# Performance work log

Measured on AMD Instinct MI355X. Metric: run time of the kernel, lower is better.

## Reference

```python
import jax, jax.numpy as jnp
import numpy as np

T, C, A = 8192, 512, 64  # context_length, embedding_size, attention_size
EPS = 1e-5


def setup_inputs() -> dict:
    key = jax.random.key(0)
    ks = jax.random.split(key, 5)
    x = jax.random.normal(ks[0], (T, C), dtype=jnp.float32)
    x_emb = jax.random.normal(ks[1], (T, C), dtype=jnp.float32)
    Wq = jax.random.normal(ks[2], (C, A), dtype=jnp.float32) / np.sqrt(C)
    Wk = jax.random.normal(ks[3], (C, A), dtype=jnp.float32) / np.sqrt(C)
    Wv = jax.random.normal(ks[4], (C, C), dtype=jnp.float32) / np.sqrt(C)
    return {
        "x": x,
        "x_emb": x_emb,
        "ln_scale": jnp.ones((C,), jnp.float32),
        "ln_bias": jnp.zeros((C,), jnp.float32),
        "Wq": Wq,
        "Wk": Wk,
        "Wv": Wv,
    }


def _layernorm(x, scale, bias):
    mu = jnp.mean(x, axis=-1, keepdims=True)
    var = jnp.mean(jnp.square(x - mu), axis=-1, keepdims=True)
    return (x - mu) * jax.lax.rsqrt(var + EPS) * scale + bias


def reference(x, x_emb, ln_scale, ln_bias, Wq, Wk, Wv):
    t = x.shape[0]
    xx = _layernorm(x, ln_scale, ln_bias)            # [T, C]
    q = xx @ Wq                                       # [T, A]
    k = xx @ Wk                                       # [T, A]
    c = jnp.einsum('ta,sa->ts', q, k) * (A ** -0.5)  # [T, T]
    # causal tril mask; masked positions set to 0 (NO softmax in this module)
    mask = jnp.tril(jnp.ones((t, t), dtype=bool))
    c = jnp.where(mask, c, 0.0)
    v = x_emb @ Wv                                    # [T, C]
    return x + c @ v
```

## Files before the change

kernel.cpp:

```cpp
#include <hip/hip_runtime.h>

#define TT 8192
#define CC 512

typedef unsigned short u16;
typedef unsigned int u32;
typedef __attribute__((ext_vector_type(8))) short bf16x8;
typedef __attribute__((ext_vector_type(4))) float f32x4;

#define VMCNT0() asm volatile("s_waitcnt vmcnt(0)" ::: "memory")
#define LGKM0()  asm volatile("s_waitcnt lgkmcnt(0)" ::: "memory")

__device__ __forceinline__ u16 f2bf(float f) {
    u32 u = __float_as_uint(f);
    return (u16)((u + 0x7FFFu + ((u >> 16) & 1u)) >> 16);
}

__device__ __forceinline__ void gld16(const u16* g, u16* l) {
    __builtin_amdgcn_global_load_lds(
        (const __attribute__((address_space(1))) u32*)g,
        (__attribute__((address_space(3))) u32*)l, 16, 0, 0);
}

__global__ void lnw_kernel(const float* __restrict__ x,
                           const float* __restrict__ scale,
                           const float* __restrict__ bias,
                           const float* __restrict__ Wq,
                           const float* __restrict__ Wk,
                           const float* __restrict__ Wv,
                           const float* __restrict__ xe,
                           u16* __restrict__ xx,
                           u16* __restrict__ wqkt,
                           u16* __restrict__ wvt,
                           u16* __restrict__ xeb) {
    int b = blockIdx.x;
    if (b < 2048) {
        int row = b * 4 + (threadIdx.x >> 6);
        int l = threadIdx.x & 63;
        const float4* xr = (const float4*)(x + (size_t)row * CC);
        float4 a = xr[l * 2], c = xr[l * 2 + 1];
        float s = a.x + a.y + a.z + a.w + c.x + c.y + c.z + c.w;
        float q = a.x*a.x + a.y*a.y + a.z*a.z + a.w*a.w
                + c.x*c.x + c.y*c.y + c.z*c.z + c.w*c.w;
        #pragma unroll
        for (int m = 1; m < 64; m <<= 1) {
            s += __shfl_xor(s, m, 64);
            q += __shfl_xor(q, m, 64);
        }
        float mu = s * (1.0f / CC);
        float var = q * (1.0f / CC) - mu * mu;
        float rs = rsqrtf(var + 1e-5f);
        const float4* sc4 = (const float4*)scale;
        const float4* bi4 = (const float4*)bias;
        float4 s1 = sc4[l * 2], s2 = sc4[l * 2 + 1];
        float4 b1 = bi4[l * 2], b2 = bi4[l * 2 + 1];
        bf16x8 o;
        o[0] = (short)f2bf((a.x - mu) * rs * s1.x + b1.x);
        o[1] = (short)f2bf((a.y - mu) * rs * s1.y + b1.y);
        o[2] = (short)f2bf((a.z - mu) * rs * s1.z + b1.z);
        o[3] = (short)f2bf((a.w - mu) * rs * s1.w + b1.w);
        o[4] = (short)f2bf((c.x - mu) * rs * s2.x + b2.x);
        o[5] = (short)f2bf((c.y - mu) * rs * s2.y + b2.y);
        o[6] = (short)f2bf((c.z - mu) * rs * s2.z + b2.z);
        o[7] = (short)f2bf((c.w - mu) * rs * s2.w + b2.w);
        *(bf16x8*)(xx + (size_t)row * CC + l * 8) = o;
    } else if (b < 3328) {
        int tid = (b - 2048) * 256 + threadIdx.x;
        if (tid < 65536) {
            int c = tid >> 9, k = tid & 511;
            float w = (c < 64) ? Wq[k * 64 + c] * 0.125f : Wk[k * 64 + (c - 64)];
            wqkt[tid] = f2bf(w);
        } else {
            int i = tid - 65536;
            int c = i >> 9, k = i & 511;
            wvt[i] = f2bf(Wv[k * 512 + c]);
        }
    } else {
        size_t i = (size_t)(b - 3328) * 2048 + (size_t)threadIdx.x * 8;
        float4 a = *(const float4*)(xe + i);
        float4 c = *(const float4*)(xe + i + 4);
        bf16x8 o;
        o[0] = (short)f2bf(a.x); o[1] = (short)f2bf(a.y);
        o[2] = (short)f2bf(a.z); o[3] = (short)f2bf(a.w);
        o[4] = (short)f2bf(c.x); o[5] = (short)f2bf(c.y);
        o[6] = (short)f2bf(c.z); o[7] = (short)f2bf(c.w);
        *(bf16x8*)(xeb + i) = o;
    }
}

__global__ __launch_bounds__(512, 4) void qkv_gemm_kernel(const u16* __restrict__ xx,
                                                          const u16* __restrict__ wqkt,
                                                          const u16* __restrict__ xeb,
                                                          const u16* __restrict__ wvt,
                                                          u16* __restrict__ qk,
                                                          u16* __restrict__ kt,
                                                          u16* __restrict__ vt) {
    extern __shared__ u16 smem[];

    const int tid = threadIdx.x;
    const int w = tid >> 6, l = tid & 63;
    const int l15 = l & 15, g = l >> 4;
    const int wr = w >> 2, wc = w & 3;

    const bool isqk = blockIdx.x < 64;
    int r0, c0;
    const u16 *Asrc, *Bsrc;
    if (isqk) { r0 = blockIdx.x * 128; c0 = 0; Asrc = xx; Bsrc = wqkt; }
    else {
        int b2 = blockIdx.x - 64;
        r0 = (b2 >> 2) * 128; c0 = (b2 & 3) * 128; Asrc = xeb; Bsrc = wvt;
    }

    const int drow = tid >> 3, sl = tid & 7;
    #define A_DMA(KK, B) { \
        _Pragma("unroll") \
        for (int i = 0; i < 2; ++i) { \
            int r = i * 64 + drow; \
            gld16(Asrc + (size_t)(r0 + r) * CC + (KK) * 64 + ((sl ^ (r & 7)) << 3), \
                  smem + (B) * 8192 + r * 64 + sl * 8); \
        } }
    #define B_DMA(KK, B) { \
        _Pragma("unroll") \
        for (int i = 0; i < 2; ++i) { \
            int r = i * 64 + drow; \
            gld16(Bsrc + (size_t)(c0 + r) * CC + (KK) * 64 + ((sl ^ (r & 7)) << 3), \
                  smem + 16384 + (B) * 8192 + r * 64 + sl * 8); \
        } }

    f32x4 acc[4][2];
    #pragma unroll
    for (int m = 0; m < 4; ++m)
        #pragma unroll
        for (int n = 0; n < 2; ++n) acc[m][n] = (f32x4){0.f, 0.f, 0.f, 0.f};

    A_DMA(0, 0); B_DMA(0, 0);

    int cur = 0;
    for (int kk = 0; kk < 8; ++kk) {
        VMCNT0();
        LGKM0();
        __builtin_amdgcn_s_barrier();
        if (kk < 7) { A_DMA(kk + 1, cur ^ 1); B_DMA(kk + 1, cur ^ 1); }

        const u16* Ab = smem + cur * 8192;
        const u16* Bb = smem + 16384 + cur * 8192;
        __builtin_amdgcn_s_setprio(1);
        #pragma unroll
        for (int ka = 0; ka < 2; ++ka) {
            bf16x8 af[4], bfr[2];
            #pragma unroll
            for (int Mt = 0; Mt < 4; ++Mt) {
                int r = wr * 64 + Mt * 16 + l15;
                int ph = (ka * 4 + g) ^ (r & 7);
                af[Mt] = *(const bf16x8*)&Ab[r * 64 + ph * 8];
            }
            #pragma unroll
            for (int Nt = 0; Nt < 2; ++Nt) {
                int c = wc * 32 + Nt * 16 + l15;
                int ph = (ka * 4 + g) ^ (c & 7);
                bfr[Nt] = *(const bf16x8*)&Bb[c * 64 + ph * 8];
            }
            #pragma unroll
            for (int Mt = 0; Mt < 4; ++Mt)
                #pragma unroll
                for (int Nt = 0; Nt < 2; ++Nt)
                    acc[Mt][Nt] = __builtin_amdgcn_mfma_f32_16x16x32_bf16(af[Mt], bfr[Nt], acc[Mt][Nt], 0, 0, 0);
        }
        __builtin_amdgcn_s_setprio(0);
        cur ^= 1;
    }

    if (isqk) {
        #pragma unroll
        for (int Mt = 0; Mt < 4; ++Mt) {
            #pragma unroll
            for (int Nt = 0; Nt < 2; ++Nt) {
                int col = wc * 32 + Nt * 16 + l15;
                #pragma unroll
                for (int jj = 0; jj < 4; ++jj) {
                    int row = wr * 64 + Mt * 16 + g * 4 + jj;
                    qk[(size_t)(r0 + row) * 128 + col] = f2bf(acc[Mt][Nt][jj]);
                }
            }
        }
        __syncthreads();
        u16* tl = smem;
        if (wc >= 2) {
            #pragma unroll
            for (int Mt = 0; Mt < 4; ++Mt) {
                #pragma unroll
                for (int Nt = 0; Nt < 2; ++Nt) {
                    int a = (wc - 2) * 32 + Nt * 16 + l15;
                    #pragma unroll
                    for (int jj = 0; jj < 4; ++jj) {
                        int row = wr * 64 + Mt * 16 + g * 4 + jj;
                        tl[a * 136 + row] = f2bf(acc[Mt][Nt][jj]);
                    }
                }
            }
        }
        __syncthreads();
        #pragma unroll
        for (int i = 0; i < 2; ++i) {
            int chunk = i * 512 + tid;
            int a = chunk >> 4, r8 = chunk & 15;
            *(bf16x8*)(kt + (size_t)a * TT + r0 + r8 * 8) = *(const bf16x8*)&tl[a * 136 + r8 * 8];
        }
    } else {
        __syncthreads();
        u16* tl = smem;
        #pragma unroll
        for (int Mt = 0; Mt < 4; ++Mt) {
            #pragma unroll
            for (int Nt = 0; Nt < 2; ++Nt) {
                int col = wc * 32 + Nt * 16 + l15;
                #pragma unroll
                for (int jj = 0; jj < 4; ++jj) {
                    int row = wr * 64 + Mt * 16 + g * 4 + jj;
                    tl[col * 136 + row] = f2bf(acc[Mt][Nt][jj]);
                }
            }
        }
        __syncthreads();
        #pragma unroll
        for (int i = 0; i < 4; ++i) {
            int chunk = i * 512 + tid;
            int c = chunk >> 4, r8 = chunk & 15;
            *(bf16x8*)(vt + (size_t)(c0 + c) * TT + r0 + r8 * 8) = *(const bf16x8*)&tl[c * 136 + r8 * 8];
        }
    }
    #undef A_DMA
    #undef B_DMA
}

__global__ __launch_bounds__(512) void gkv_kernel(const u16* __restrict__ vt,
                                                  const u16* __restrict__ kt,
                                                  float* __restrict__ H) {
    int m = blockIdx.x >> 2, cq = blockIdx.x & 3;
    int w = threadIdx.x >> 6, l = threadIdx.x & 63;
    int l15 = l & 15, g = l >> 4;
    int c0 = cq * 128 + (w >> 1) * 32;
    int a0 = (w & 1) * 32;

    f32x4 acc[2][2];
    #pragma unroll
    for (int i = 0; i < 2; ++i)
        #pragma unroll
        for (int n = 0; n < 2; ++n) acc[i][n] = (f32x4){0.f, 0.f, 0.f, 0.f};

    #pragma unroll
    for (int ka = 0; ka < 4; ++ka) {
        int k = m * 128 + ka * 32 + g * 8;
        bf16x8 af[2], bfr[2];
        #pragma unroll
        for (int Mt = 0; Mt < 2; ++Mt)
            af[Mt] = *(const bf16x8*)(vt + (size_t)(c0 + Mt * 16 + l15) * TT + k);
        #pragma unroll
        for (int Nt = 0; Nt < 2; ++Nt)
            bfr[Nt] = *(const bf16x8*)(kt + (size_t)(a0 + Nt * 16 + l15) * TT + k);
        #pragma unroll
        for (int Mt = 0; Mt < 2; ++Mt)
            #pragma unroll
            for (int Nt = 0; Nt < 2; ++Nt)
                acc[Mt][Nt] = __builtin_amdgcn_mfma_f32_16x16x32_bf16(af[Mt], bfr[Nt], acc[Mt][Nt], 0, 0, 0);
    }

    float* hp = H + (size_t)m * 32768;
    #pragma unroll
    for (int Mt = 0; Mt < 2; ++Mt) {
        #pragma unroll
        for (int Nt = 0; Nt < 2; ++Nt) {
            int a = a0 + Nt * 16 + l15;
            #pragma unroll
            for (int jj = 0; jj < 4; ++jj) {
                int c = c0 + Mt * 16 + g * 4 + jj;
                hp[c * 64 + a] = acc[Mt][Nt][jj];
            }
        }
    }
}

__global__ __launch_bounds__(256) void scanA_kernel(const float* __restrict__ H,
                                                    float* __restrict__ Asum) {
    int idx = blockIdx.x * 256 + threadIdx.x;
    int g = idx >> 15, e = idx & 32767;
    float s = 0.f;
    #pragma unroll
    for (int t = 0; t < 8; ++t) s += H[(size_t)(8 * g + t) * 32768 + e];
    Asum[(size_t)g * 32768 + e] = s;
}

__global__ __launch_bounds__(256) void scanB_kernel(const float* __restrict__ H,
                                                    const float* __restrict__ Asum,
                                                    u16* __restrict__ ptb) {
    int idx = blockIdx.x * 256 + threadIdx.x;
    int g = idx >> 15, e = idx & 32767;
    float acc = 0.f;
    for (int g2 = 0; g2 < g; ++g2) acc += Asum[(size_t)g2 * 32768 + e];
    ptb[(size_t)(8 * g) * 32768 + e] = f2bf(acc);
    #pragma unroll
    for (int t = 1; t < 8; ++t) {
        acc += H[(size_t)(8 * g + t - 1) * 32768 + e];
        ptb[(size_t)(8 * g + t) * 32768 + e] = f2bf(acc);
    }
}

__global__ __launch_bounds__(512) void out_kernel(const u16* __restrict__ qk,
                                                  const u16* __restrict__ ptb,
                                                  const u16* __restrict__ vt,
                                                  const float* __restrict__ x,
                                                  float* __restrict__ out) {
    __shared__ u16 Slds[128 * 128];

    const int tid = threadIdx.x;
    const int w = tid >> 6, l = tid & 63;
    const int l15 = l & 15, g = l >> 4;
    const int wr = w >> 2, wcol = w & 3;

    const int rt = (int)blockIdx.x >> 2;
    const int cb = (int)blockIdx.x & 3;

    f32x4 acc[4][2];
    #pragma unroll
    for (int m = 0; m < 4; ++m)
        #pragma unroll
        for (int n = 0; n < 2; ++n) acc[m][n] = (f32x4){0.f, 0.f, 0.f, 0.f};

    const int dq = rt * 128 + w * 16 + l15;
    const bf16x8 qa0 = *(const bf16x8*)(qk + (size_t)dq * 128 + g * 8);
    const bf16x8 qa1 = *(const bf16x8*)(qk + (size_t)dq * 128 + 32 + g * 8);
    #pragma unroll
    for (int Nt = 0; Nt < 8; ++Nt) {
        int scol = Nt * 16 + l15;
        f32x4 sacc = (f32x4){0.f, 0.f, 0.f, 0.f};
        #pragma unroll
        for (int ka = 0; ka < 2; ++ka) {
            bf16x8 kf = *(const bf16x8*)(qk + (size_t)(rt * 128 + scol) * 128 + 64 + ka * 32 + g * 8);
            sacc = __builtin_amdgcn_mfma_f32_16x16x32_bf16(ka ? qa1 : qa0, kf, sacc, 0, 0, 0);
        }
        #pragma unroll
        for (int jj = 0; jj < 4; ++jj) {
            int row = w * 16 + g * 4 + jj;
            float val = (scol > row) ? 0.f : sacc[jj];
            int slot = (scol >> 3) ^ (row & 15);
            Slds[row * 128 + slot * 8 + (scol & 7)] = f2bf(val);
        }
    }

    #pragma unroll
    for (int ka = 0; ka < 2; ++ka) {
        bf16x8 qf[4], pf[2];
        #pragma unroll
        for (int Mt = 0; Mt < 4; ++Mt)
            qf[Mt] = *(const bf16x8*)(qk + (size_t)(rt * 128 + wr * 64 + Mt * 16 + l15) * 128 + ka * 32 + g * 8);
        #pragma unroll
        for (int Nt = 0; Nt < 2; ++Nt) {
            int c = cb * 128 + wcol * 32 + Nt * 16 + l15;
            pf[Nt] = *(const bf16x8*)(ptb + (size_t)rt * 32768 + c * 64 + ka * 32 + g * 8);
        }
        #pragma unroll
        for (int Mt = 0; Mt < 4; ++Mt)
            #pragma unroll
            for (int Nt = 0; Nt < 2; ++Nt)
                acc[Mt][Nt] = __builtin_amdgcn_mfma_f32_16x16x32_bf16(qf[Mt], pf[Nt], acc[Mt][Nt], 0, 0, 0);
    }

    __syncthreads();

    #pragma unroll
    for (int ks = 0; ks < 4; ++ks) {
        bf16x8 sf[4], vf[2];
        #pragma unroll
        for (int Mt = 0; Mt < 4; ++Mt) {
            int row = wr * 64 + Mt * 16 + l15;
            int slot = (ks * 4 + g) ^ (row & 15);
            sf[Mt] = *(const bf16x8*)&Slds[row * 128 + slot * 8];
        }
        #pragma unroll
        for (int Nt = 0; Nt < 2; ++Nt) {
            int c = cb * 128 + wcol * 32 + Nt * 16 + l15;
            vf[Nt] = *(const bf16x8*)(vt + (size_t)c * TT + rt * 128 + ks * 32 + g * 8);
        }
        #pragma unroll
        for (int Mt = 0; Mt < 4; ++Mt)
            #pragma unroll
            for (int Nt = 0; Nt < 2; ++Nt)
                acc[Mt][Nt] = __builtin_amdgcn_mfma_f32_16x16x32_bf16(sf[Mt], vf[Nt], acc[Mt][Nt], 0, 0, 0);
    }

    #pragma unroll
    for (int Mt = 0; Mt < 4; ++Mt) {
        #pragma unroll
        for (int Nt = 0; Nt < 2; ++Nt) {
            int col = cb * 128 + wcol * 32 + Nt * 16 + l15;
            #pragma unroll
            for (int jj = 0; jj < 4; ++jj) {
                int row = rt * 128 + wr * 64 + Mt * 16 + g * 4 + jj;
                out[(size_t)row * 512 + col] = x[(size_t)row * 512 + col] + acc[Mt][Nt][jj];
            }
        }
    }
}

extern "C" void kernel_launch(void* const* d_in, const int* in_sizes, int n_in,
                              void* d_out, int out_size, void* d_ws, size_t ws_size,
                              hipStream_t stream) {
    (void)in_sizes; (void)n_in; (void)out_size; (void)ws_size;
    const float* x    = (const float*)d_in[0];
    const float* xe   = (const float*)d_in[1];
    const float* lns  = (const float*)d_in[2];
    const float* lnb  = (const float*)d_in[3];
    const float* Wq   = (const float*)d_in[4];
    const float* Wk   = (const float*)d_in[5];
    const float* Wv   = (const float*)d_in[6];
    float* out = (float*)d_out;
    char* ws = (char*)d_ws;

    size_t off_xx   = 0;
    size_t off_qk   = off_xx   + (size_t)TT * CC * 2;
    size_t off_wqkt = off_qk   + (size_t)TT * 128 * 2;
    size_t off_wvt  = off_wqkt + (size_t)128 * 512 * 2;
    size_t off_vt   = off_wvt  + (size_t)512 * 512 * 2;
    size_t off_xeb  = off_vt   + (size_t)TT * CC * 2;
    size_t off_kt   = off_xeb  + (size_t)TT * CC * 2;
    size_t off_h    = off_kt   + (size_t)64 * TT * 2;
    size_t off_as   = off_h    + (size_t)64 * 32768 * 4;
    size_t off_ptb  = off_as   + (size_t)8 * 32768 * 4;

    u16* xx   = (u16*)(ws + off_xx);
    u16* qk   = (u16*)(ws + off_qk);
    u16* wqkt = (u16*)(ws + off_wqkt);
    u16* wvt  = (u16*)(ws + off_wvt);
    u16* vt   = (u16*)(ws + off_vt);
    u16* xeb  = (u16*)(ws + off_xeb);
    u16* kt   = (u16*)(ws + off_kt);
    float* H  = (float*)(ws + off_h);
    float* As = (float*)(ws + off_as);
    u16* ptb  = (u16*)(ws + off_ptb);

    const size_t qkv_lds = 65536;

    hipLaunchKernelGGL(lnw_kernel,      dim3(5376), dim3(256), 0, stream,
                       x, lns, lnb, Wq, Wk, Wv, xe, xx, wqkt, wvt, xeb);
    hipLaunchKernelGGL(qkv_gemm_kernel, dim3(320),  dim3(512), qkv_lds, stream,
                       xx, wqkt, xeb, wvt, qk, kt, vt);
    hipLaunchKernelGGL(gkv_kernel,      dim3(256),  dim3(512), 0, stream, vt, kt, H);
    hipLaunchKernelGGL(scanA_kernel,    dim3(1024), dim3(256), 0, stream, H, As);
    hipLaunchKernelGGL(scanB_kernel,    dim3(1024), dim3(256), 0, stream, H, As, ptb);
    hipLaunchKernelGGL(out_kernel,      dim3(256),  dim3(512), 0, stream, qk, ptb, vt, x, out);
}
```

Baseline: 54.29 us.

## Fuse per-chunk KV outer-product GEMM with group sum into one kernel

Merges the gkv kernel that computes per-chunk K^T V partial products with the scanA kernel that sums groups of eight chunks. Each block now loops over eight consecutive chunks for a 64-column slice and accumulates the group sum in registers, writing both H and Asum. This removes a kernel launch and the re-read of H for the group sums. The cost is a grid of only 64 blocks with a serial loop per block, which lowers parallelism and latency hiding on a large GPU.

```diff
diff --git a/kernel.cpp b/kernel.cpp
--- a/kernel.cpp
+++ b/kernel.cpp
@@ -233,61 +233,57 @@
     #undef B_DMA
 }
 
-__global__ __launch_bounds__(512) void gkv_kernel(const u16* __restrict__ vt,
-                                                  const u16* __restrict__ kt,
-                                                  float* __restrict__ H) {
-    int m = blockIdx.x >> 2, cq = blockIdx.x & 3;
+__global__ __launch_bounds__(512) void gkvA_kernel(const u16* __restrict__ vt,
+                                                   const u16* __restrict__ kt,
+                                                   float* __restrict__ H,
+                                                   float* __restrict__ Asum) {
+    int g = blockIdx.x >> 3, cs = blockIdx.x & 7;
     int w = threadIdx.x >> 6, l = threadIdx.x & 63;
-    int l15 = l & 15, g = l >> 4;
-    int c0 = cq * 128 + (w >> 1) * 32;
+    int l15 = l & 15, g16 = l >> 4;
+    int c0 = cs * 64 + (w >> 1) * 16;
     int a0 = (w & 1) * 32;
 
-    f32x4 acc[2][2];
-    #pragma unroll
-    for (int i = 0; i < 2; ++i)
-        #pragma unroll
-        for (int n = 0; n < 2; ++n) acc[i][n] = (f32x4){0.f, 0.f, 0.f, 0.f};
-
-    #pragma unroll
-    for (int ka = 0; ka < 4; ++ka) {
-        int k = m * 128 + ka * 32 + g * 8;
-        bf16x8 af[2], bfr[2];
-        #pragma unroll
-        for (int Mt = 0; Mt < 2; ++Mt)
-            af[Mt] = *(const bf16x8*)(vt + (size_t)(c0 + Mt * 16 + l15) * TT + k);
-        #pragma unroll
-        for (int Nt = 0; Nt < 2; ++Nt)
-            bfr[Nt] = *(const bf16x8*)(kt + (size_t)(a0 + Nt * 16 + l15) * TT + k);
-        #pragma unroll
-        for (int Mt = 0; Mt < 2; ++Mt)
-            #pragma unroll
-            for (int Nt = 0; Nt < 2; ++Nt)
-                acc[Mt][Nt] = __builtin_amdgcn_mfma_f32_16x16x32_bf16(af[Mt], bfr[Nt], acc[Mt][Nt], 0, 0, 0);
-    }
-
-    float* hp = H + (size_t)m * 32768;
-    #pragma unroll
-    for (int Mt = 0; Mt < 2; ++Mt) {
+    f32x4 asum[2];
+    asum[0] = (f32x4){0.f, 0.f, 0.f, 0.f};
+    asum[1] = (f32x4){0.f, 0.f, 0.f, 0.f};
+
+    for (int t = 0; t < 8; ++t) {
+        int m = g * 8 + t;
+        f32x4 facc[2];
+        facc[0] = (f32x4){0.f, 0.f, 0.f, 0.f};
+        facc[1] = (f32x4){0.f, 0.f, 0.f, 0.f};
+        #pragma unroll
+        for (int ka = 0; ka < 4; ++ka) {
+            int k = m * 128 + ka * 32 + g16 * 8;
+            bf16x8 af = *(const bf16x8*)(vt + (size_t)(c0 + l15) * TT + k);
+            #pragma unroll
+            for (int Nt = 0; Nt < 2; ++Nt) {
+                bf16x8 bfr = *(const bf16x8*)(kt + (size_t)(a0 + Nt * 16 + l15) * TT + k);
+                facc[Nt] = __builtin_amdgcn_mfma_f32_16x16x32_bf16(af, bfr, facc[Nt], 0, 0, 0);
+            }
+        }
+        float* hp = H + (size_t)m * 32768;
         #pragma unroll
         for (int Nt = 0; Nt < 2; ++Nt) {
             int a = a0 + Nt * 16 + l15;
             #pragma unroll
             for (int jj = 0; jj < 4; ++jj) {
-                int c = c0 + Mt * 16 + g * 4 + jj;
-                hp[c * 64 + a] = acc[Mt][Nt][jj];
-            }
-        }
-    }
-}
-
-__global__ __launch_bounds__(256) void scanA_kernel(const float* __restrict__ H,
-                                                    float* __restrict__ Asum) {
-    int idx = blockIdx.x * 256 + threadIdx.x;
-    int g = idx >> 15, e = idx & 32767;
-    float s = 0.f;
-    #pragma unroll
-    for (int t = 0; t < 8; ++t) s += H[(size_t)(8 * g + t) * 32768 + e];
-    Asum[(size_t)g * 32768 + e] = s;
+                int c = c0 + g16 * 4 + jj;
+                hp[c * 64 + a] = facc[Nt][jj];
+                asum[Nt][jj] += facc[Nt][jj];
+            }
+        }
+    }
+    float* ap = Asum + (size_t)g * 32768;
+    #pragma unroll
+    for (int Nt = 0; Nt < 2; ++Nt) {
+        int a = a0 + Nt * 16 + l15;
+        #pragma unroll
+        for (int jj = 0; jj < 4; ++jj) {
+            int c = c0 + g16 * 4 + jj;
+            ap[c * 64 + a] = asum[Nt][jj];
+        }
+    }
 }
 
 __global__ __launch_bounds__(256) void scanB_kernel(const float* __restrict__ H,
@@ -444,8 +440,7 @@
                        x, lns, lnb, Wq, Wk, Wv, xe, xx, wqkt, wvt, xeb);
     hipLaunchKernelGGL(qkv_gemm_kernel, dim3(320),  dim3(512), qkv_lds, stream,
                        xx, wqkt, xeb, wvt, qk, kt, vt);
-    hipLaunchKernelGGL(gkv_kernel,      dim3(256),  dim3(512), 0, stream, vt, kt, H);
-    hipLaunchKernelGGL(scanA_kernel,    dim3(1024), dim3(256), 0, stream, H, As);
+    hipLaunchKernelGGL(gkvA_kernel,     dim3(64),   dim3(512), 0, stream, vt, kt, H, As);
     hipLaunchKernelGGL(scanB_kernel,    dim3(1024), dim3(256), 0, stream, H, As, ptb);
     hipLaunchKernelGGL(out_kernel,      dim3(256),  dim3(512), 0, stream, qk, ptb, vt, x, out);
 }
```

New measurement: 70.65 us. +30.1%, slower.
